# Kernel optimization log

Measured on AMD Instinct MI355X. Metric: run time of the kernel, lower is better.

The kernel has to match this reference:

```python
import jax, jax.numpy as jnp
import numpy as np

D_IN, D_OUT, RANK, N = 4096, 4096, 16, 8192


def _quantize_weight(w, bits):
    # round-to-nearest fake quantization, stored back as floats (as in the torch code)
    absmax = jnp.abs(w).max()
    scale = (2 ** (bits - 1) - 1) / absmax
    q = jnp.clip(jnp.round(w * scale), -2 ** (bits - 1), 2 ** (bits - 1) - 1)
    return q / scale


def _double_quantization(w, bits):
    absmax = jnp.abs(w).max()
    c1 = (2 ** (bits - 1) - 1) / absmax          # scalar fp32 scale
    q = jnp.clip(jnp.round(w * c1), -2 ** (bits - 1), 2 ** (bits - 1) - 1)
    return c1, q / c1                             # c_kbit_2 has same shape as w


def setup_inputs() -> dict:
    key = jax.random.key(0)
    kX, kW, kL1, kL2 = jax.random.split(key, 4)
    X = jax.random.normal(kX, (N, D_IN), dtype=jnp.float32)
    W0 = jax.random.normal(kW, (D_IN, D_OUT), dtype=jnp.float32)
    W_nf4 = _quantize_weight(W0, bits=4)
    c_fp32_1, c_kbit_2 = _double_quantization(W_nf4, bits=8)
    L1 = jax.random.normal(kL1, (D_IN, RANK), dtype=jnp.float32)
    L2 = jax.random.normal(kL2, (RANK, D_OUT), dtype=jnp.float32)
    return {"X": X, "W_nf4": W_nf4, "c_fp32_1": c_fp32_1,
            "c_kbit_2": c_kbit_2, "L1": L1, "L2": L2}


def reference(X, W_nf4, c_fp32_1, c_kbit_2, L1, L2):
    # dequantize: elementwise scalar * elementwise-tensor scaling of stored weight
    W = W_nf4 * c_fp32_1 * c_kbit_2               # [D_IN, D_OUT]
    # main GEMM + low-rank LoRA path, added in the epilogue
    Y = X @ W + (X @ L1) @ L2                     # [N, D_OUT]
    return Y
```

## Files before the change

### kernel.cpp

```cpp
#include <hip/hip_runtime.h>


#define M_ROWS 8192
#define K_DIM  4096
#define N_OUT  4096
#define XL1_BLOCKS 512
#define WP_BLOCKS  4096

typedef float  f32x16 __attribute__((ext_vector_type(16)));
typedef float  f32x4  __attribute__((ext_vector_type(4)));
typedef __bf16 bf16x8 __attribute__((ext_vector_type(8)));
typedef unsigned short ushort8v __attribute__((ext_vector_type(8)));

__device__ float          Tg[(size_t)M_ROWS * 16];
__device__ unsigned short L1t[16 * K_DIM];
__device__ unsigned short L2t[N_OUT * 16];

__device__ __forceinline__ unsigned short f2bf(float f) {
    __bf16 h = (__bf16)f;
    union { __bf16 h; unsigned short u; } v; v.h = h;
    return v.u;
}

__global__ __launch_bounds__(256) void lorap_kernel(
        const float* __restrict__ L1, const float* __restrict__ L2) {
    const int idx = blockIdx.x * 256 + threadIdx.x;
    if (idx < K_DIM) {
        const float4* lp = (const float4*)&L1[(size_t)idx * 16];
        float4 r0 = lp[0], r1 = lp[1], r2 = lp[2], r3 = lp[3];
        float v[16] = {r0.x, r0.y, r0.z, r0.w, r1.x, r1.y, r1.z, r1.w,
                       r2.x, r2.y, r2.z, r2.w, r3.x, r3.y, r3.z, r3.w};
        #pragma unroll
        for (int r = 0; r < 16; ++r)
            L1t[(size_t)r * K_DIM + idx] = f2bf(v[r]);
    } else {
        const int n = idx - K_DIM;
        ushort8v a, b;
        #pragma unroll
        for (int r = 0; r < 8; ++r) a[r] = f2bf(L2[(size_t)r * N_OUT + n]);
        #pragma unroll
        for (int r = 0; r < 8; ++r) b[r] = f2bf(L2[(size_t)(r + 8) * N_OUT + n]);
        *(ushort8v*)&L2t[(size_t)n * 16]     = a;
        *(ushort8v*)&L2t[(size_t)n * 16 + 8] = b;
    }
}

__global__ __launch_bounds__(256) void prep_all_kernel(
        const float* __restrict__ X,    unsigned short* __restrict__ Xh,
        const float* __restrict__ Wnf4, const float* __restrict__ c1p,
        const float* __restrict__ c2,   unsigned short* __restrict__ Wt) {
    const int t = threadIdx.x;

    if (blockIdx.x < XL1_BLOCKS) {
        __shared__ float red[4][256];
        const int m0 = blockIdx.x * 16;
        const int wv = t >> 6, lane = t & 63;
        const int l15 = lane & 15, l4 = lane >> 4;
        const size_t rowoff = (size_t)(m0 + l15) * K_DIM + wv * 1024 + l4 * 8;
        const float* ap = X + rowoff;
        unsigned short* xp = Xh + rowoff;
        const __bf16* bp = (const __bf16*)L1t + (size_t)l15 * K_DIM + wv * 1024 + l4 * 8;
        f32x4 acc = {};
        #pragma unroll 8
        for (int k = 0; k < 1024; k += 32) {
            float4 p0 = *(const float4*)(ap + k);
            float4 p1 = *(const float4*)(ap + k + 4);
            bf16x8 a;
            a[0] = (__bf16)p0.x; a[1] = (__bf16)p0.y;
            a[2] = (__bf16)p0.z; a[3] = (__bf16)p0.w;
            a[4] = (__bf16)p1.x; a[5] = (__bf16)p1.y;
            a[6] = (__bf16)p1.z; a[7] = (__bf16)p1.w;
            *(bf16x8*)(xp + k) = a;
            bf16x8 b = *(const bf16x8*)(bp + k);
            acc = __builtin_amdgcn_mfma_f32_16x16x32_bf16(a, b, acc, 0, 0, 0);
        }
        #pragma unroll
        for (int r = 0; r < 4; ++r) red[wv][(l4 * 4 + r) * 16 + l15] = acc[r];
        __syncthreads();
        if (wv == 0) {
            #pragma unroll
            for (int r = 0; r < 4; ++r) {
                int e = (l4 * 4 + r) * 16 + l15;
                Tg[(size_t)(m0 + l4 * 4 + r) * 16 + l15] =
                    red[0][e] + red[1][e] + red[2][e] + red[3][e];
            }
        }
        return;
    }

    {
        __shared__ unsigned short tile[64][72];
        const int wb = blockIdx.x - XL1_BLOCKS;
        const int n0 = (wb & 63) * 64;
        const int k0 = (wb >> 6) * 64;
        const float c1 = *c1p;

        #pragma unroll
        for (int i = 0; i < 4; ++i) {
            int idx = i * 1024 + t * 4;
            int k = idx >> 6, n4 = idx & 63;
            size_t g = (size_t)(k0 + k) * N_OUT + n0 + n4;
            float4 w = *(const float4*)&Wnf4[g];
            float4 s = *(const float4*)&c2[g];
            tile[n4    ][k] = f2bf(w.x * c1 * s.x);
            tile[n4 + 1][k] = f2bf(w.y * c1 * s.y);
            tile[n4 + 2][k] = f2bf(w.z * c1 * s.z);
            tile[n4 + 3][k] = f2bf(w.w * c1 * s.w);
        }
        __syncthreads();

        #pragma unroll
        for (int i = 0; i < 2; ++i) {
            int task = i * 256 + t;
            int n = task >> 3, k8 = (task & 7) * 8;
            ushort8v o = *(const ushort8v*)&tile[n][k8];
            *(ushort8v*)&Wt[(size_t)(n0 + n) * K_DIM + k0 + k8] = o;
        }
    }
}

#define COMPUTE(B) do { \
    bf16x8 af[2][2], bfr[2][2]; \
    _Pragma("unroll") for (int mt = 0; mt < 2; ++mt) \
      _Pragma("unroll") for (int ks = 0; ks < 2; ++ks) { \
        int row = wm + mt * 32 + l32; \
        int slot = (2 * ks + half) ^ rsw; \
        af[mt][ks] = *(const bf16x8*)(&As[B][0] + row * 32 + slot * 8); \
      } \
    _Pragma("unroll") for (int nt = 0; nt < 2; ++nt) \
      _Pragma("unroll") for (int ks = 0; ks < 2; ++ks) { \
        int row = wn + nt * 32 + l32; \
        int slot = (2 * ks + half) ^ rsw; \
        bfr[nt][ks] = *(const bf16x8*)(&Bs[B][0] + row * 32 + slot * 8); \
      } \
    _Pragma("unroll") for (int ks = 0; ks < 2; ++ks) \
      _Pragma("unroll") for (int mt = 0; mt < 2; ++mt) \
        _Pragma("unroll") for (int nt = 0; nt < 2; ++nt) \
          acc[mt][nt] = __builtin_amdgcn_mfma_f32_32x32x16_bf16( \
              af[mt][ks], bfr[nt][ks], acc[mt][nt], 0, 0, 0); \
} while (0)

__global__ __launch_bounds__(256) void gemm_bt_kernel(
        const __bf16* __restrict__ A, const __bf16* __restrict__ Bt,
        float* __restrict__ C, int m_base) {
    __shared__ __bf16 As[2][128 * 32];
    __shared__ __bf16 Bs[2][128 * 32];

    const int t    = threadIdx.x;
    const int w    = t >> 6;
    const int lane = t & 63;
    const int half = lane >> 5;
    const int l32  = lane & 31;

    const int m0   = m_base + blockIdx.y * 128;
    const int n0   = blockIdx.x * 128;

    const int wm   = (w >> 1) * 64;
    const int wn   = (w & 1) * 64;

    const int srow = lane >> 2;
    const int scol = ((lane & 3) ^ ((lane >> 3) & 3)) * 8;
    const int rsw = (l32 >> 1) & 3;

    f32x16 acc[2][2] = {};

    for (int kb = 0; kb < K_DIM; kb += 64) {
        __syncthreads();
        #pragma unroll
        for (int b = 0; b < 2; ++b) {
            #pragma unroll
            for (int j = 0; j < 2; ++j) {
                int row = w * 32 + j * 16 + srow;
                const __bf16* gp = A + (size_t)(m0 + row) * K_DIM + kb + b * 32 + scol;
                __builtin_amdgcn_global_load_lds(
                    (const __attribute__((address_space(1))) unsigned int*)gp,
                    (__attribute__((address_space(3))) unsigned int*)
                        (&As[b][0] + (w * 32 + j * 16) * 32),
                    16, 0, 0);
            }
            #pragma unroll
            for (int j = 0; j < 2; ++j) {
                int row = w * 32 + j * 16 + srow;
                const __bf16* gp = Bt + (size_t)(n0 + row) * K_DIM + kb + b * 32 + scol;
                __builtin_amdgcn_global_load_lds(
                    (const __attribute__((address_space(1))) unsigned int*)gp,
                    (__attribute__((address_space(3))) unsigned int*)
                        (&Bs[b][0] + (w * 32 + j * 16) * 32),
                    16, 0, 0);
            }
        }
        __syncthreads();

        COMPUTE(0);
        COMPUTE(1);
    }

    {
        bf16x8 afl[2], bfl[2];
        #pragma unroll
        for (int mt = 0; mt < 2; ++mt) {
            const float* tp = Tg + (size_t)(m0 + wm + mt * 32 + l32) * 16 + half * 8;
            float4 p0 = *(const float4*)tp;
            float4 p1 = *(const float4*)(tp + 4);
            afl[mt][0] = (__bf16)p0.x; afl[mt][1] = (__bf16)p0.y;
            afl[mt][2] = (__bf16)p0.z; afl[mt][3] = (__bf16)p0.w;
            afl[mt][4] = (__bf16)p1.x; afl[mt][5] = (__bf16)p1.y;
            afl[mt][6] = (__bf16)p1.z; afl[mt][7] = (__bf16)p1.w;
        }
        #pragma unroll
        for (int nt = 0; nt < 2; ++nt)
            bfl[nt] = *(const bf16x8*)((const __bf16*)L2t +
                        (size_t)(n0 + wn + nt * 32 + l32) * 16 + half * 8);
        #pragma unroll
        for (int mt = 0; mt < 2; ++mt)
            #pragma unroll
            for (int nt = 0; nt < 2; ++nt)
                acc[mt][nt] = __builtin_amdgcn_mfma_f32_32x32x16_bf16(
                    afl[mt], bfl[nt], acc[mt][nt], 0, 0, 0);
    }

    #pragma unroll
    for (int mt = 0; mt < 2; ++mt)
        #pragma unroll
        for (int nt = 0; nt < 2; ++nt) {
            int col = n0 + wn + nt * 32 + l32;
            #pragma unroll
            for (int reg = 0; reg < 16; ++reg) {
                int row = m0 + wm + mt * 32 + (reg & 3) + 8 * (reg >> 2) + 4 * half;
                C[(size_t)row * N_OUT + col] = acc[mt][nt][reg];
            }
        }
}

extern "C" void kernel_launch(void* const* d_in, const int* in_sizes, int n_in,
                              void* d_out, int out_size, void* d_ws, size_t ws_size,
                              hipStream_t stream) {
    const float* X    = (const float*)d_in[0];
    const float* Wnf4 = (const float*)d_in[1];
    const float* c1   = (const float*)d_in[2];
    const float* c2   = (const float*)d_in[3];
    const float* L1   = (const float*)d_in[4];
    const float* L2   = (const float*)d_in[5];
    float* Y = (float*)d_out;

    unsigned short* Xh = (unsigned short*)d_ws;
    unsigned short* Wt = (unsigned short*)((char*)d_ws + (size_t)M_ROWS * K_DIM * 2);

    lorap_kernel<<<32, 256, 0, stream>>>(L1, L2);
    prep_all_kernel<<<XL1_BLOCKS + WP_BLOCKS, 256, 0, stream>>>(
        X, Xh, Wnf4, c1, c2, Wt);

    gemm_bt_kernel<<<dim3(N_OUT / 128, 32), 256, 0, stream>>>(
        (const __bf16*)Xh, (const __bf16*)Wt, Y, 0);
    gemm_bt_kernel<<<dim3(N_OUT / 128, 32), 256, 0, stream>>>(
        (const __bf16*)Xh, (const __bf16*)Wt, Y, 4096);
}
```

Baseline: 636.3 us.

## Software-pipeline GEMM main loop so global-to-LDS loads overlap MFMA

Restructures the GEMM K-loop into a rolling two-stage pipeline over 32-wide K tiles. After fragments are read from the current LDS buffer, the global_load_lds for tile t+2 into that same buffer is issued before the MFMAs run. Explicit s_waitcnt and raw s_barrier calls replace __syncthreads so that load latency hides behind compute. This adds more barriers per K step and relies on manual waitcnt counts being exactly right, which is a correctness risk if the count of outstanding loads per tile is miscounted.

Result: slower. 650.7 us (+2.3%).

```diff
diff --git a/kernel.cpp b/kernel.cpp
--- a/kernel.cpp
+++ b/kernel.cpp
@@ -6,6 +6,7 @@
 #define N_OUT  4096
 #define XL1_BLOCKS 512
 #define WP_BLOCKS  4096
+#define NTILES 128
 
 typedef float  f32x16 __attribute__((ext_vector_type(16)));
 typedef float  f32x4  __attribute__((ext_vector_type(4)));
@@ -119,8 +120,27 @@
     }
 }
 
-#define COMPUTE(B) do { \
-    bf16x8 af[2][2], bfr[2][2]; \
+#define FBAR() do { asm volatile("" ::: "memory"); \
+    __builtin_amdgcn_s_barrier(); asm volatile("" ::: "memory"); } while (0)
+
+#define STG(B, KS) do { \
+    const int kb_ = (KS) * 32; \
+    _Pragma("unroll") for (int j = 0; j < 2; ++j) { \
+        int row = w * 32 + j * 16 + srow; \
+        const __bf16* ga = A + (size_t)(m0 + row) * K_DIM + kb_ + scol; \
+        __builtin_amdgcn_global_load_lds( \
+            (const __attribute__((address_space(1))) unsigned int*)ga, \
+            (__attribute__((address_space(3))) unsigned int*) \
+                (&As[B][0] + (w * 32 + j * 16) * 32), 16, 0, 0); \
+        const __bf16* gb = Bt + (size_t)(n0 + row) * K_DIM + kb_ + scol; \
+        __builtin_amdgcn_global_load_lds( \
+            (const __attribute__((address_space(1))) unsigned int*)gb, \
+            (__attribute__((address_space(3))) unsigned int*) \
+                (&Bs[B][0] + (w * 32 + j * 16) * 32), 16, 0, 0); \
+    } \
+} while (0)
+
+#define LOAD_FRAGS(B) do { \
     _Pragma("unroll") for (int mt = 0; mt < 2; ++mt) \
       _Pragma("unroll") for (int ks = 0; ks < 2; ++ks) { \
         int row = wm + mt * 32 + l32; \
@@ -133,6 +153,9 @@
         int slot = (2 * ks + half) ^ rsw; \
         bfr[nt][ks] = *(const bf16x8*)(&Bs[B][0] + row * 32 + slot * 8); \
       } \
+} while (0)
+
+#define DO_MFMA() do { \
     _Pragma("unroll") for (int ks = 0; ks < 2; ++ks) \
       _Pragma("unroll") for (int mt = 0; mt < 2; ++mt) \
         _Pragma("unroll") for (int nt = 0; nt < 2; ++nt) \
@@ -163,37 +186,31 @@
     const int rsw = (l32 >> 1) & 3;
 
     f32x16 acc[2][2] = {};
-
-    for (int kb = 0; kb < K_DIM; kb += 64) {
-        __syncthreads();
-        #pragma unroll
-        for (int b = 0; b < 2; ++b) {
-            #pragma unroll
-            for (int j = 0; j < 2; ++j) {
-                int row = w * 32 + j * 16 + srow;
-                const __bf16* gp = A + (size_t)(m0 + row) * K_DIM + kb + b * 32 + scol;
-                __builtin_amdgcn_global_load_lds(
-                    (const __attribute__((address_space(1))) unsigned int*)gp,
-                    (__attribute__((address_space(3))) unsigned int*)
-                        (&As[b][0] + (w * 32 + j * 16) * 32),
-                    16, 0, 0);
-            }
-            #pragma unroll
-            for (int j = 0; j < 2; ++j) {
-                int row = w * 32 + j * 16 + srow;
-                const __bf16* gp = Bt + (size_t)(n0 + row) * K_DIM + kb + b * 32 + scol;
-                __builtin_amdgcn_global_load_lds(
-                    (const __attribute__((address_space(1))) unsigned int*)gp,
-                    (__attribute__((address_space(3))) unsigned int*)
-                        (&Bs[b][0] + (w * 32 + j * 16) * 32),
-                    16, 0, 0);
-            }
-        }
-        __syncthreads();
-
-        COMPUTE(0);
-        COMPUTE(1);
-    }
+    bf16x8 af[2][2], bfr[2][2];
+
+    STG(0, 0);
+    STG(1, 1);
+    asm volatile("s_waitcnt vmcnt(4)" ::: "memory");
+    FBAR();
+
+    for (int tt = 0; tt < NTILES - 2; ++tt) {
+        const int cur = tt & 1;
+        LOAD_FRAGS(cur);
+        asm volatile("s_waitcnt lgkmcnt(0)" ::: "memory");
+        FBAR();
+        STG(cur, tt + 2);
+        DO_MFMA();
+        asm volatile("s_waitcnt vmcnt(4)" ::: "memory");
+        FBAR();
+    }
+    LOAD_FRAGS(0);
+    asm volatile("s_waitcnt lgkmcnt(0)" ::: "memory");
+    FBAR();
+    DO_MFMA();
+    asm volatile("s_waitcnt vmcnt(0)" ::: "memory");
+    FBAR();
+    LOAD_FRAGS(1);
+    DO_MFMA();
 
     {
         bf16x8 afl[2], bfl[2];
```
